# Kernel tuning notes

Hardware: AMD Instinct MI355X
Metric: run time of the kernel (lower is better)

Reference implementation:

```python
import jax, jax.numpy as jnp
import numpy as np

HEADS = 8
EMB = 128

def setup_inputs() -> dict:
    key = jax.random.key(0)
    ks = jax.random.split(key, 5)
    b, t, hin = 4, 128, 1024
    N = 50000
    x = jax.random.normal(ks[0], (b, t, hin), dtype=jnp.float32)
    curiosity_score = jax.random.normal(ks[1], (b, t), dtype=jnp.float32)
    Wq = jax.random.normal(ks[2], (EMB * HEADS, hin), dtype=jnp.float32) * (1.0 / np.sqrt(hin))
    keys = jax.random.normal(ks[3], (N, EMB), dtype=jnp.float32)
    values = jax.random.normal(ks[4], (N,), dtype=jnp.float32)
    return {"x": x, "curiosity_score": curiosity_score, "Wq": Wq, "keys": keys, "values": values}

def reference(x, curiosity_score, Wq, keys, values):
    b, t, hin = x.shape
    h, e = HEADS, EMB
    # query projection (torch Linear, no bias): x @ Wq.T -> (b, t, h*e)
    q = jnp.einsum('bti,oi->bto', x, Wq).reshape(b, t, h, e)
    q = q / (e ** 0.25)
    # scores vs shared offline key bank (N, e); buffer was `heads` identical copies,
    # so broadcasting over h is the same math without materializing repeats.
    scores = jnp.einsum('bthe,ne->bthn', q, keys)          # (b, t, h, N)
    attn = jax.nn.softmax(scores, axis=-1)
    # weighted sum of scalar values; curiosity adds a per-query constant to every
    # value, and since attn rows sum to 1 this equals adding curiosity afterwards.
    out = jnp.einsum('bthn,n->bth', attn, values) + curiosity_score[:, :, None]
    out = out.mean(axis=2)                                  # mean over heads
    return out[:, :, None]                                  # (b, t, 1)
```

## Files before the change

kernel.cpp:

```cpp
#include <hip/hip_runtime.h>

#define NHEADS   8
#define EMB_     128
#define BT_      512
#define HIN_     1024
#define NQ_      4096
#define NKEY_    50000
#define NGRP_REAL_ 3125
#define NGRP_    3200
#define NPAD_    51200
#define NPADKEYS_ 1200.0f
#define GPS_     50
#define NSLICES_ 64

#define PROJB_   512
#define CONVB_   1024

#define QSCALE   (0.29730177875068026f * 1.4426950408889634f)

typedef __attribute__((ext_vector_type(8))) short short8v;
typedef __attribute__((ext_vector_type(4))) float float4v;

#if __has_builtin(__builtin_amdgcn_exp2f)
#define EXP2F(x) __builtin_amdgcn_exp2f(x)
#else
#define EXP2F(x) exp2f(x)
#endif

__device__ __forceinline__ short f2bf(float f) {
  unsigned u = __float_as_uint(f);
  u += 0x7fffu + ((u >> 16) & 1u);
  return (short)(u >> 16);
}

#if __has_builtin(__builtin_amdgcn_cvt_pk_bf16_f32)
typedef __attribute__((ext_vector_type(2))) __bf16 bf16x2;
__device__ __forceinline__ unsigned pk2(float a, float b) {
  bf16x2 r = __builtin_amdgcn_cvt_pk_bf16_f32(a, b);
  union { bf16x2 v; unsigned u; } c; c.v = r; return c.u;
}
#else
__device__ __forceinline__ unsigned pk2(float a, float b) {
  return (unsigned)(unsigned short)f2bf(a) | ((unsigned)(unsigned short)f2bf(b) << 16);
}
#endif

__global__ __launch_bounds__(256) void prep_kernel(
    const float* __restrict__ x, const float* __restrict__ Wq,
    short* __restrict__ qb,
    const float* __restrict__ keys, const float* __restrict__ values,
    short* __restrict__ keys_fr, float* __restrict__ vpad) {
  if (blockIdx.x < PROJB_) {
    const int wave = threadIdx.x >> 6, lane = threadIdx.x & 63;
    const int quad = lane >> 4, ln = lane & 15;
    const int tile = blockIdx.x * 4 + wave;
    const int mt = tile >> 6, ot = tile & 63;
    const float* xrow = x  + (mt * 16 + ln) * HIN_ + quad * 8;
    const float* wrow = Wq + (ot * 16 + ln) * HIN_ + quad * 8;
    float4v d = {0.f, 0.f, 0.f, 0.f};

    float4 xa0 = *(const float4*)(xrow);
    float4 xa1 = *(const float4*)(xrow + 4);
    float4 wa0 = *(const float4*)(wrow);
    float4 wa1 = *(const float4*)(wrow + 4);
    float4 xb0 = *(const float4*)(xrow + 32);
    float4 xb1 = *(const float4*)(xrow + 36);
    float4 wb0 = *(const float4*)(wrow + 32);
    float4 wb1 = *(const float4*)(wrow + 36);

#pragma unroll 1
    for (int k0 = 0; k0 < HIN_; k0 += 64) {
      union { short8v s8; unsigned u[4]; } af, bf;
      af.u[0] = pk2(xa0.x, xa0.y); af.u[1] = pk2(xa0.z, xa0.w);
      af.u[2] = pk2(xa1.x, xa1.y); af.u[3] = pk2(xa1.z, xa1.w);
      bf.u[0] = pk2(wa0.x, wa0.y); bf.u[1] = pk2(wa0.z, wa0.w);
      bf.u[2] = pk2(wa1.x, wa1.y); bf.u[3] = pk2(wa1.z, wa1.w);
      if (k0 + 64 < HIN_) {
        xa0 = *(const float4*)(xrow + k0 + 64);
        xa1 = *(const float4*)(xrow + k0 + 68);
        wa0 = *(const float4*)(wrow + k0 + 64);
        wa1 = *(const float4*)(wrow + k0 + 68);
      }
      d = __builtin_amdgcn_mfma_f32_16x16x32_bf16(af.s8, bf.s8, d, 0, 0, 0);

      af.u[0] = pk2(xb0.x, xb0.y); af.u[1] = pk2(xb0.z, xb0.w);
      af.u[2] = pk2(xb1.x, xb1.y); af.u[3] = pk2(xb1.z, xb1.w);
      bf.u[0] = pk2(wb0.x, wb0.y); bf.u[1] = pk2(wb0.z, wb0.w);
      bf.u[2] = pk2(wb1.x, wb1.y); bf.u[3] = pk2(wb1.z, wb1.w);
      if (k0 + 96 < HIN_) {
        xb0 = *(const float4*)(xrow + k0 + 96);
        xb1 = *(const float4*)(xrow + k0 + 100);
        wb0 = *(const float4*)(wrow + k0 + 96);
        wb1 = *(const float4*)(wrow + k0 + 100);
      }
      d = __builtin_amdgcn_mfma_f32_16x16x32_bf16(af.s8, bf.s8, d, 0, 0, 0);
    }
#pragma unroll
    for (int r2 = 0; r2 < 4; ++r2)
      qb[(mt * 16 + quad * 4 + r2) * HIN_ + ot * 16 + ln] = f2bf(d[r2] * QSCALE);
  } else {
    const int cb = blockIdx.x - PROJB_;
    const int t  = threadIdx.x;
#pragma unroll 1
    for (int g = cb; g < NGRP_; g += CONVB_) {
      if (g < NGRP_REAL_) {
        const float* src = keys + (g * 16 + (t & 15)) * EMB_ + (t >> 4) * 8;
        float4 v0 = ((const float4*)src)[0];
        float4 v1 = ((const float4*)src)[1];
        union { short8v s8; unsigned u[4]; } o;
        o.u[0] = pk2(v0.x, v0.y); o.u[1] = pk2(v0.z, v0.w);
        o.u[2] = pk2(v1.x, v1.y); o.u[3] = pk2(v1.z, v1.w);
        ((short8v*)keys_fr)[g * 256 + t] = o.s8;
        if (t < 16) vpad[g * 16 + t] = values[g * 16 + t];
      } else {
        short8v z = (short8v)0;
        ((short8v*)keys_fr)[g * 256 + t] = z;
        if (t < 16) vpad[g * 16 + t] = 0.f;
      }
    }
  }
}

__global__ __launch_bounds__(256) void attn_kernel(
    const short* __restrict__ qb,
    const short* __restrict__ keys_fr,
    const float* __restrict__ vpad,
    float* __restrict__ partials) {
  const int t     = threadIdx.x;
  const int wave  = t >> 6;
  const int lane  = t & 63;
  const int quad  = lane >> 4;
  const int ln    = lane & 15;
  const int l     = blockIdx.x;
  const int xcd   = l & 7;
  const int j     = l >> 3;
  const int slice = xcd * 8 + (j >> 4);
  const int chunk = j & 15;
  const int qbase = chunk * 256 + wave * 64;
  const int g0    = slice * GPS_;
  const int g1    = g0 + GPS_;

  short8v a[4][4];
#pragma unroll
  for (int sub = 0; sub < 4; ++sub)
#pragma unroll
    for (int ks = 0; ks < 4; ++ks)
      a[sub][ks] = *(const short8v*)(qb + (qbase + sub * 16 + ln) * EMB_ + ks * 32 + quad * 8);

  float lsum[4][4], asum[4][4];
#pragma unroll
  for (int i = 0; i < 4; ++i)
#pragma unroll
    for (int jj = 0; jj < 4; ++jj) { lsum[i][jj] = 0.f; asum[i][jj] = 0.f; }

  short8v bA[4], bB[4];
  float vA, vB;
#pragma unroll
  for (int ks = 0; ks < 4; ++ks)
    bA[ks] = *(const short8v*)(keys_fr + ((g0 * 4 + ks) * 64 + lane) * 8);
  vA = vpad[g0 * 16 + ln];
#pragma unroll
  for (int ks = 0; ks < 4; ++ks)
    bB[ks] = *(const short8v*)(keys_fr + (((g0 + 1) * 4 + ks) * 64 + lane) * 8);
  vB = vpad[(g0 + 1) * 16 + ln];

#pragma unroll 1
  for (int g = g0; g < g1; g += 2) {
    {
      float4v d[4];
#pragma unroll
      for (int sub = 0; sub < 4; ++sub) d[sub] = (float4v){0.f, 0.f, 0.f, 0.f};
      __builtin_amdgcn_s_setprio(1);
#pragma unroll
      for (int ks = 0; ks < 4; ++ks)
#pragma unroll
        for (int sub = 0; sub < 4; ++sub)
          d[sub] = __builtin_amdgcn_mfma_f32_16x16x32_bf16(a[sub][ks], bA[ks], d[sub], 0, 0, 0);
      __builtin_amdgcn_s_setprio(0);
      if (g + 2 < g1) {
#pragma unroll
        for (int ks = 0; ks < 4; ++ks)
          bA[ks] = *(const short8v*)(keys_fr + (((g + 2) * 4 + ks) * 64 + lane) * 8);
      }
      float vv = vA;
      if (g + 2 < g1) vA = vpad[(g + 2) * 16 + ln];
#pragma unroll
      for (int sub = 0; sub < 4; ++sub)
#pragma unroll
        for (int r2 = 0; r2 < 4; ++r2) {
          float p = EXP2F(d[sub][r2]);
          lsum[sub][r2] += p;
          asum[sub][r2] = fmaf(p, vv, asum[sub][r2]);
        }
    }
    {
      float4v d[4];
#pragma unroll
      for (int sub = 0; sub < 4; ++sub) d[sub] = (float4v){0.f, 0.f, 0.f, 0.f};
      __builtin_amdgcn_s_setprio(1);
#pragma unroll
      for (int ks = 0; ks < 4; ++ks)
#pragma unroll
        for (int sub = 0; sub < 4; ++sub)
          d[sub] = __builtin_amdgcn_mfma_f32_16x16x32_bf16(a[sub][ks], bB[ks], d[sub], 0, 0, 0);
      __builtin_amdgcn_s_setprio(0);
      if (g + 3 < g1) {
#pragma unroll
        for (int ks = 0; ks < 4; ++ks)
          bB[ks] = *(const short8v*)(keys_fr + (((g + 3) * 4 + ks) * 64 + lane) * 8);
      }
      float vv = vB;
      if (g + 3 < g1) vB = vpad[(g + 3) * 16 + ln];
#pragma unroll
      for (int sub = 0; sub < 4; ++sub)
#pragma unroll
        for (int r2 = 0; r2 < 4; ++r2) {
          float p = EXP2F(d[sub][r2]);
          lsum[sub][r2] += p;
          asum[sub][r2] = fmaf(p, vv, asum[sub][r2]);
        }
    }
  }

#pragma unroll
  for (int sub = 0; sub < 4; ++sub)
#pragma unroll
    for (int r2 = 0; r2 < 4; ++r2) {
      float L = lsum[sub][r2], A = asum[sub][r2];
#pragma unroll
      for (int m = 1; m < 16; m <<= 1) {
        L += __shfl_xor(L, m, 64);
        A += __shfl_xor(A, m, 64);
      }
      if (ln == 0) {
        int q = qbase + sub * 16 + quad * 4 + r2;
        partials[(q * NSLICES_ + slice) * 2 + 0] = L;
        partials[(q * NSLICES_ + slice) * 2 + 1] = A;
      }
    }
}

__global__ __launch_bounds__(256) void finalize_kernel(
    const float* __restrict__ partials, const float* __restrict__ cur,
    float* __restrict__ out) {
  int tid = blockIdx.x * 256 + threadIdx.x;
  int bt = tid >> 3, h = tid & 7;
  int q = bt * NHEADS + h;
  const float4* p = (const float4*)(partials + q * NSLICES_ * 2);
  float sl = 0.f, sa = 0.f;
#pragma unroll
  for (int i = 0; i < NSLICES_ / 2; ++i) {
    float4 v = p[i];
    sl += v.x + v.z;
    sa += v.y + v.w;
  }
  sl -= NPADKEYS_;
  float r = sa / sl;
  r += __shfl_xor(r, 1, 64);
  r += __shfl_xor(r, 2, 64);
  r += __shfl_xor(r, 4, 64);
  if (h == 0) out[bt] = r * (1.f / NHEADS) + cur[bt];
}

extern "C" void kernel_launch(void* const* d_in, const int* in_sizes, int n_in,
                              void* d_out, int out_size, void* d_ws, size_t ws_size,
                              hipStream_t stream) {
  (void)in_sizes; (void)n_in; (void)out_size; (void)ws_size;
  const float* x      = (const float*)d_in[0];
  const float* cur    = (const float*)d_in[1];
  const float* Wq     = (const float*)d_in[2];
  const float* keys   = (const float*)d_in[3];
  const float* values = (const float*)d_in[4];
  float* out = (float*)d_out;

  char* ws = (char*)d_ws;
  short* keys_fr = (short*)(ws);
  float* vpad    = (float*)(ws + 13107200);
  short* qb      = (short*)(ws + 13312000);
  float* part    = (float*)(ws + 14360576);

  hipLaunchKernelGGL(prep_kernel, dim3(PROJB_ + CONVB_), dim3(256), 0, stream,
                     x, Wq, qb, keys, values, keys_fr, vpad);
  hipLaunchKernelGGL(attn_kernel, dim3(1024), dim3(256), 0, stream,
                     qb, keys_fr, vpad, part);
  hipLaunchKernelGGL(finalize_kernel, dim3(16), dim3(256), 0, stream, part, cur, out);
}
```

Baseline: 175.0 us.

## Compute softmax sums and value-weighted sums with an extra MFMA

The per-element scalar accumulation (lsum += p, asum += p*v) is replaced by a second MFMA. Exponentiated scores from two key groups are packed to bf16 and multiplied by a value fragment whose lanes carry the values split into bf16 hi/lo parts plus a ones-vector for the normalizer. The score MFMA operands are swapped so the output layout feeds this MFMA directly, and the cross-lane shuffle reductions at the end are dropped. This removes VALU FMA work and reductions from the hot loop. In exchange the probabilities are rounded to bf16 before accumulation, which adds precision risk and an extra per-iteration load of the value fragment.

```diff
diff --git a/kernel.cpp b/kernel.cpp
--- a/kernel.cpp
+++ b/kernel.cpp
@@ -8,7 +8,7 @@
 #define NKEY_    50000
 #define NGRP_REAL_ 3125
 #define NGRP_    3200
-#define NPAD_    51200
+#define NPAIR_   1600
 #define NPADKEYS_ 1200.0f
 #define GPS_     50
 #define NSLICES_ 64
@@ -32,6 +32,9 @@
   u += 0x7fffu + ((u >> 16) & 1u);
   return (short)(u >> 16);
 }
+__device__ __forceinline__ float bf2f(short h) {
+  return __uint_as_float(((unsigned)(unsigned short)h) << 16);
+}
 
 #if __has_builtin(__builtin_amdgcn_cvt_pk_bf16_f32)
 typedef __attribute__((ext_vector_type(2))) __bf16 bf16x2;
@@ -41,7 +44,9 @@
 }
 #else
 __device__ __forceinline__ unsigned pk2(float a, float b) {
-  return (unsigned)(unsigned short)f2bf(a) | ((unsigned)(unsigned short)f2bf(b) << 16);
+  unsigned r;
+  asm("v_cvt_pk_bf16_f32 %0, %1, %2" : "=v"(r) : "v"(a), "v"(b));
+  return r;
 }
 #endif
 
@@ -49,7 +54,7 @@
     const float* __restrict__ x, const float* __restrict__ Wq,
     short* __restrict__ qb,
     const float* __restrict__ keys, const float* __restrict__ values,
-    short* __restrict__ keys_fr, float* __restrict__ vpad) {
+    short* __restrict__ keys_fr, short* __restrict__ vfr) {
   if (blockIdx.x < PROJB_) {
     const int wave = threadIdx.x >> 6, lane = threadIdx.x & 63;
     const int quad = lane >> 4, ln = lane & 15;
@@ -111,12 +116,27 @@
         o.u[0] = pk2(v0.x, v0.y); o.u[1] = pk2(v0.z, v0.w);
         o.u[2] = pk2(v1.x, v1.y); o.u[3] = pk2(v1.z, v1.w);
         ((short8v*)keys_fr)[g * 256 + t] = o.s8;
-        if (t < 16) vpad[g * 16 + t] = values[g * 16 + t];
       } else {
         short8v z = (short8v)0;
         ((short8v*)keys_fr)[g * 256 + t] = z;
-        if (t < 16) vpad[g * 16 + t] = 0.f;
       }
+    }
+    const int wi = cb * 256 + t;
+    if (wi < NPAIR_ * 4) {
+      const int pg = wi >> 2, Q = wi & 3;
+      short hi[8], lo[8];
+#pragma unroll
+      for (int e = 0; e < 4; ++e) {
+        int idxE = pg * 32 + Q * 4 + e;
+        int idxO = idxE + 16;
+        float fE = (idxE < NKEY_) ? values[idxE] : 0.f;
+        float fO = (idxO < NKEY_) ? values[idxO] : 0.f;
+        hi[e]     = f2bf(fE); lo[e]     = f2bf(fE - bf2f(hi[e]));
+        hi[4 + e] = f2bf(fO); lo[4 + e] = f2bf(fO - bf2f(hi[4 + e]));
+      }
+      short* dst = vfr + pg * 64 + Q * 16;
+#pragma unroll
+      for (int e = 0; e < 8; ++e) { dst[e] = hi[e]; dst[8 + e] = lo[e]; }
     }
   }
 }
@@ -124,7 +144,7 @@
 __global__ __launch_bounds__(256) void attn_kernel(
     const short* __restrict__ qb,
     const short* __restrict__ keys_fr,
-    const float* __restrict__ vpad,
+    const short* __restrict__ vfr,
     float* __restrict__ partials) {
   const int t     = threadIdx.x;
   const int wave  = t >> 6;
@@ -147,97 +167,94 @@
     for (int ks = 0; ks < 4; ++ks)
       a[sub][ks] = *(const short8v*)(qb + (qbase + sub * 16 + ln) * EMB_ + ks * 32 + quad * 8);
 
-  float lsum[4][4], asum[4][4];
-#pragma unroll
-  for (int i = 0; i < 4; ++i)
-#pragma unroll
-    for (int jj = 0; jj < 4; ++jj) { lsum[i][jj] = 0.f; asum[i][jj] = 0.f; }
+  float4v dpv[4];
+#pragma unroll
+  for (int sub = 0; sub < 4; ++sub) dpv[sub] = (float4v){0.f, 0.f, 0.f, 0.f};
+
+  const bool datalane = (ln == 0) || (ln == 2);
+  const unsigned cvf = (ln == 1) ? 0x3F803F80u : 0u;
+  const unsigned vinv = datalane ? (unsigned)(quad * 16 + (ln == 2 ? 8 : 0)) : 0u;
+  const unsigned dmask = datalane ? 0xFFFFFFFFu : 0u;
 
   short8v bA[4], bB[4];
-  float vA, vB;
 #pragma unroll
   for (int ks = 0; ks < 4; ++ks)
     bA[ks] = *(const short8v*)(keys_fr + ((g0 * 4 + ks) * 64 + lane) * 8);
-  vA = vpad[g0 * 16 + ln];
 #pragma unroll
   for (int ks = 0; ks < 4; ++ks)
     bB[ks] = *(const short8v*)(keys_fr + (((g0 + 1) * 4 + ks) * 64 + lane) * 8);
-  vB = vpad[(g0 + 1) * 16 + ln];
 
 #pragma unroll 1
   for (int g = g0; g < g1; g += 2) {
-    {
-      float4v d[4];
-#pragma unroll
-      for (int sub = 0; sub < 4; ++sub) d[sub] = (float4v){0.f, 0.f, 0.f, 0.f};
-      __builtin_amdgcn_s_setprio(1);
+    union { short8v s8; unsigned u[4]; } vfu, vlu;
+    vlu.s8 = *(const short8v*)(vfr + (vinv + (((unsigned)((g >> 1) * 64)) & dmask)));
+#pragma unroll
+    for (int i = 0; i < 4; ++i) vfu.u[i] = datalane ? vlu.u[i] : cvf;
+
+    float4v dE[4], dO[4];
+#pragma unroll
+    for (int sub = 0; sub < 4; ++sub) dE[sub] = (float4v){0.f, 0.f, 0.f, 0.f};
+    __builtin_amdgcn_s_setprio(1);
+#pragma unroll
+    for (int ks = 0; ks < 4; ++ks)
+#pragma unroll
+      for (int sub = 0; sub < 4; ++sub)
+        dE[sub] = __builtin_amdgcn_mfma_f32_16x16x32_bf16(bA[ks], a[sub][ks], dE[sub], 0, 0, 0);
+    __builtin_amdgcn_s_setprio(0);
+    if (g + 2 < g1) {
 #pragma unroll
       for (int ks = 0; ks < 4; ++ks)
-#pragma unroll
-        for (int sub = 0; sub < 4; ++sub)
-          d[sub] = __builtin_amdgcn_mfma_f32_16x16x32_bf16(a[sub][ks], bA[ks], d[sub], 0, 0, 0);
-      __builtin_amdgcn_s_setprio(0);
-      if (g + 2 < g1) {
-#pragma unroll
-        for (int ks = 0; ks < 4; ++ks)
-          bA[ks] = *(const short8v*)(keys_fr + (((g + 2) * 4 + ks) * 64 + lane) * 8);
-      }
-      float vv = vA;
-      if (g + 2 < g1) vA = vpad[(g + 2) * 16 + ln];
+        bA[ks] = *(const short8v*)(keys_fr + (((g + 2) * 4 + ks) * 64 + lane) * 8);
+    }
+#pragma unroll
+    for (int sub = 0; sub < 4; ++sub)
+#pragma unroll
+      for (int r2 = 0; r2 < 4; ++r2) dE[sub][r2] = EXP2F(dE[sub][r2]);
+    unsigned pbl[4][2];
+#pragma unroll
+    for (int sub = 0; sub < 4; ++sub) {
+      pbl[sub][0] = pk2(dE[sub][0], dE[sub][1]);
+      pbl[sub][1] = pk2(dE[sub][2], dE[sub][3]);
+    }
+
+#pragma unroll
+    for (int sub = 0; sub < 4; ++sub) dO[sub] = (float4v){0.f, 0.f, 0.f, 0.f};
+    __builtin_amdgcn_s_setprio(1);
+#pragma unroll
+    for (int ks = 0; ks < 4; ++ks)
 #pragma unroll
       for (int sub = 0; sub < 4; ++sub)
-#pragma unroll
-        for (int r2 = 0; r2 < 4; ++r2) {
-          float p = EXP2F(d[sub][r2]);
-          lsum[sub][r2] += p;
-          asum[sub][r2] = fmaf(p, vv, asum[sub][r2]);
-        }
-    }
-    {
-      float4v d[4];
-#pragma unroll
-      for (int sub = 0; sub < 4; ++sub) d[sub] = (float4v){0.f, 0.f, 0.f, 0.f};
-      __builtin_amdgcn_s_setprio(1);
+        dO[sub] = __builtin_amdgcn_mfma_f32_16x16x32_bf16(bB[ks], a[sub][ks], dO[sub], 0, 0, 0);
+    __builtin_amdgcn_s_setprio(0);
+    if (g + 3 < g1) {
 #pragma unroll
       for (int ks = 0; ks < 4; ++ks)
-#pragma unroll
-        for (int sub = 0; sub < 4; ++sub)
-          d[sub] = __builtin_amdgcn_mfma_f32_16x16x32_bf16(a[sub][ks], bB[ks], d[sub], 0, 0, 0);
-      __builtin_amdgcn_s_setprio(0);
-      if (g + 3 < g1) {
-#pragma unroll
-        for (int ks = 0; ks < 4; ++ks)
-          bB[ks] = *(const short8v*)(keys_fr + (((g + 3) * 4 + ks) * 64 + lane) * 8);
-      }
-      float vv = vB;
-      if (g + 3 < g1) vB = vpad[(g + 3) * 16 + ln];
-#pragma unroll
-      for (int sub = 0; sub < 4; ++sub)
-#pragma unroll
-        for (int r2 = 0; r2 < 4; ++r2) {
-          float p = EXP2F(d[sub][r2]);
-          lsum[sub][r2] += p;
-          asum[sub][r2] = fmaf(p, vv, asum[sub][r2]);
-        }
+        bB[ks] = *(const short8v*)(keys_fr + (((g + 3) * 4 + ks) * 64 + lane) * 8);
+    }
+#pragma unroll
+    for (int sub = 0; sub < 4; ++sub)
+#pragma unroll
+      for (int r2 = 0; r2 < 4; ++r2) dO[sub][r2] = EXP2F(dO[sub][r2]);
+
+#pragma unroll
+    for (int sub = 0; sub < 4; ++sub) {
+      union { short8v s8; unsigned u[4]; } pb;
+      pb.u[0] = pbl[sub][0];
+      pb.u[1] = pbl[sub][1];
+      pb.u[2] = pk2(dO[sub][0], dO[sub][1]);
+      pb.u[3] = pk2(dO[sub][2], dO[sub][3]);
+      dpv[sub] = __builtin_amdgcn_mfma_f32_16x16x32_bf16(vfu.s8, pb.s8, dpv[sub], 0, 0, 0);
     }
   }
 
-#pragma unroll
-  for (int sub = 0; sub < 4; ++sub)
-#pragma unroll
-    for (int r2 = 0; r2 < 4; ++r2) {
-      float L = lsum[sub][r2], A = asum[sub][r2];
-#pragma unroll
-      for (int m = 1; m < 16; m <<= 1) {
-        L += __shfl_xor(L, m, 64);
-        A += __shfl_xor(A, m, 64);
-      }
-      if (ln == 0) {
-        int q = qbase + sub * 16 + quad * 4 + r2;
-        partials[(q * NSLICES_ + slice) * 2 + 0] = L;
-        partials[(q * NSLICES_ + slice) * 2 + 1] = A;
-      }
-    }
+  if (quad == 0) {
+#pragma unroll
+    for (int sub = 0; sub < 4; ++sub) {
+      int q = qbase + sub * 16 + ln;
+      partials[(q * NSLICES_ + slice) * 2 + 0] = dpv[sub][1];
+      partials[(q * NSLICES_ + slice) * 2 + 1] = dpv[sub][0] + dpv[sub][2];
+    }
+  }
 }
 
 __global__ __launch_bounds__(256) void finalize_kernel(
@@ -275,13 +292,13 @@
 
   char* ws = (char*)d_ws;
   short* keys_fr = (short*)(ws);
-  float* vpad    = (float*)(ws + 13107200);
+  short* vfr     = (short*)(ws + 13107200);
   short* qb      = (short*)(ws + 13312000);
   float* part    = (float*)(ws + 14360576);
 
   hipLaunchKernelGGL(prep_kernel, dim3(PROJB_ + CONVB_), dim3(256), 0, stream,
-                     x, Wq, qb, keys, values, keys_fr, vpad);
+                     x, Wq, qb, keys, values, keys_fr, vfr);
   hipLaunchKernelGGL(attn_kernel, dim3(1024), dim3(256), 0, stream,
-                     qb, keys_fr, vpad, part);
+                     qb, keys_fr, vfr, part);
   hipLaunchKernelGGL(finalize_kernel, dim3(16), dim3(256), 0, stream, part, cur, out);
 }
```

Result: slower. 193.2 us (+10.4%).

## Halve per-wave query tile and fuse even/odd key group MFMA chains

Applied to the files above, without the earlier changes.

Each wave now handles 32 queries instead of 64, so the grid doubles to 2048 blocks and register pressure per wave drops. The two key-group MFMA chains are issued together and their exp/accumulate work is merged into one loop, giving more independent MFMAs in flight. The unused pk2 fallback now uses inline asm for the bf16 convert, and an unused define is dropped. In exchange, key tiles are reloaded by twice as many waves, which raises L2/global traffic per query.

```diff
diff --git a/kernel.cpp b/kernel.cpp
--- a/kernel.cpp
+++ b/kernel.cpp
@@ -8,7 +8,6 @@
 #define NKEY_    50000
 #define NGRP_REAL_ 3125
 #define NGRP_    3200
-#define NPAD_    51200
 #define NPADKEYS_ 1200.0f
 #define GPS_     50
 #define NSLICES_ 64
@@ -41,7 +40,9 @@
 }
 #else
 __device__ __forceinline__ unsigned pk2(float a, float b) {
-  return (unsigned)(unsigned short)f2bf(a) | ((unsigned)(unsigned short)f2bf(b) << 16);
+  unsigned r;
+  asm("v_cvt_pk_bf16_f32 %0, %1, %2" : "=v"(r) : "v"(a), "v"(b));
+  return r;
 }
 #endif
 
@@ -134,24 +135,26 @@
   const int l     = blockIdx.x;
   const int xcd   = l & 7;
   const int j     = l >> 3;
-  const int slice = xcd * 8 + (j >> 4);
-  const int chunk = j & 15;
-  const int qbase = chunk * 256 + wave * 64;
+  const int slice = xcd * 8 + (j >> 5);
+  const int chunk = j & 31;
+  const int qbase = chunk * 128 + wave * 32;
   const int g0    = slice * GPS_;
   const int g1    = g0 + GPS_;
 
-  short8v a[4][4];
-#pragma unroll
-  for (int sub = 0; sub < 4; ++sub)
+  short8v a[2][4];
+#pragma unroll
+  for (int sub = 0; sub < 2; ++sub)
 #pragma unroll
     for (int ks = 0; ks < 4; ++ks)
       a[sub][ks] = *(const short8v*)(qb + (qbase + sub * 16 + ln) * EMB_ + ks * 32 + quad * 8);
 
-  float lsum[4][4], asum[4][4];
-#pragma unroll
-  for (int i = 0; i < 4; ++i)
+  float lsum[2][4], asum[2][4];
+#pragma unroll
+  for (int i = 0; i < 2; ++i)
 #pragma unroll
     for (int jj = 0; jj < 4; ++jj) { lsum[i][jj] = 0.f; asum[i][jj] = 0.f; }
+
+  const float4v z4 = {0.f, 0.f, 0.f, 0.f};
 
   short8v bA[4], bB[4];
   float vA, vB;
@@ -166,64 +169,50 @@
 
 #pragma unroll 1
   for (int g = g0; g < g1; g += 2) {
-    {
-      float4v d[4];
-#pragma unroll
-      for (int sub = 0; sub < 4; ++sub) d[sub] = (float4v){0.f, 0.f, 0.f, 0.f};
-      __builtin_amdgcn_s_setprio(1);
+    float4v dE[2], dO[2];
+    __builtin_amdgcn_s_setprio(1);
+    dE[0] = __builtin_amdgcn_mfma_f32_16x16x32_bf16(a[0][0], bA[0], z4, 0, 0, 0);
+    dE[1] = __builtin_amdgcn_mfma_f32_16x16x32_bf16(a[1][0], bA[0], z4, 0, 0, 0);
+    dO[0] = __builtin_amdgcn_mfma_f32_16x16x32_bf16(a[0][0], bB[0], z4, 0, 0, 0);
+    dO[1] = __builtin_amdgcn_mfma_f32_16x16x32_bf16(a[1][0], bB[0], z4, 0, 0, 0);
+#pragma unroll
+    for (int ks = 1; ks < 4; ++ks) {
+      dE[0] = __builtin_amdgcn_mfma_f32_16x16x32_bf16(a[0][ks], bA[ks], dE[0], 0, 0, 0);
+      dE[1] = __builtin_amdgcn_mfma_f32_16x16x32_bf16(a[1][ks], bA[ks], dE[1], 0, 0, 0);
+      dO[0] = __builtin_amdgcn_mfma_f32_16x16x32_bf16(a[0][ks], bB[ks], dO[0], 0, 0, 0);
+      dO[1] = __builtin_amdgcn_mfma_f32_16x16x32_bf16(a[1][ks], bB[ks], dO[1], 0, 0, 0);
+    }
+    __builtin_amdgcn_s_setprio(0);
+
+    if (g + 2 < g1) {
 #pragma unroll
       for (int ks = 0; ks < 4; ++ks)
-#pragma unroll
-        for (int sub = 0; sub < 4; ++sub)
-          d[sub] = __builtin_amdgcn_mfma_f32_16x16x32_bf16(a[sub][ks], bA[ks], d[sub], 0, 0, 0);
-      __builtin_amdgcn_s_setprio(0);
-      if (g + 2 < g1) {
-#pragma unroll
-        for (int ks = 0; ks < 4; ++ks)
-          bA[ks] = *(const short8v*)(keys_fr + (((g + 2) * 4 + ks) * 64 + lane) * 8);
-      }
-      float vv = vA;
-      if (g + 2 < g1) vA = vpad[(g + 2) * 16 + ln];
-#pragma unroll
-      for (int sub = 0; sub < 4; ++sub)
-#pragma unroll
-        for (int r2 = 0; r2 < 4; ++r2) {
-          float p = EXP2F(d[sub][r2]);
-          lsum[sub][r2] += p;
-          asum[sub][r2] = fmaf(p, vv, asum[sub][r2]);
-        }
-    }
-    {
-      float4v d[4];
-#pragma unroll
-      for (int sub = 0; sub < 4; ++sub) d[sub] = (float4v){0.f, 0.f, 0.f, 0.f};
-      __builtin_amdgcn_s_setprio(1);
+        bA[ks] = *(const short8v*)(keys_fr + (((g + 2) * 4 + ks) * 64 + lane) * 8);
+    }
+    float vvA = vA;
+    if (g + 2 < g1) vA = vpad[(g + 2) * 16 + ln];
+    if (g + 3 < g1) {
 #pragma unroll
       for (int ks = 0; ks < 4; ++ks)
-#pragma unroll
-        for (int sub = 0; sub < 4; ++sub)
-          d[sub] = __builtin_amdgcn_mfma_f32_16x16x32_bf16(a[sub][ks], bB[ks], d[sub], 0, 0, 0);
-      __builtin_amdgcn_s_setprio(0);
-      if (g + 3 < g1) {
-#pragma unroll
-        for (int ks = 0; ks < 4; ++ks)
-          bB[ks] = *(const short8v*)(keys_fr + (((g + 3) * 4 + ks) * 64 + lane) * 8);
-      }
-      float vv = vB;
-      if (g + 3 < g1) vB = vpad[(g + 3) * 16 + ln];
-#pragma unroll
-      for (int sub = 0; sub < 4; ++sub)
-#pragma unroll
-        for (int r2 = 0; r2 < 4; ++r2) {
-          float p = EXP2F(d[sub][r2]);
-          lsum[sub][r2] += p;
-          asum[sub][r2] = fmaf(p, vv, asum[sub][r2]);
-        }
-    }
+        bB[ks] = *(const short8v*)(keys_fr + (((g + 3) * 4 + ks) * 64 + lane) * 8);
+    }
+    float vvB = vB;
+    if (g + 3 < g1) vB = vpad[(g + 3) * 16 + ln];
+
+#pragma unroll
+    for (int sub = 0; sub < 2; ++sub)
+#pragma unroll
+      for (int r2 = 0; r2 < 4; ++r2) {
+        float pE = EXP2F(dE[sub][r2]);
+        float pO = EXP2F(dO[sub][r2]);
+        lsum[sub][r2] += pE + pO;
+        asum[sub][r2] = fmaf(pE, vvA, asum[sub][r2]);
+        asum[sub][r2] = fmaf(pO, vvB, asum[sub][r2]);
+      }
   }
 
 #pragma unroll
-  for (int sub = 0; sub < 4; ++sub)
+  for (int sub = 0; sub < 2; ++sub)
 #pragma unroll
     for (int r2 = 0; r2 < 4; ++r2) {
       float L = lsum[sub][r2], A = asum[sub][r2];
@@ -281,7 +270,7 @@
 
   hipLaunchKernelGGL(prep_kernel, dim3(PROJB_ + CONVB_), dim3(256), 0, stream,
                      x, Wq, qb, keys, values, keys_fr, vpad);
-  hipLaunchKernelGGL(attn_kernel, dim3(1024), dim3(256), 0, stream,
+  hipLaunchKernelGGL(attn_kernel, dim3(2048), dim3(256), 0, stream,
                      qb, keys_fr, vpad, part);
   hipLaunchKernelGGL(finalize_kernel, dim3(16), dim3(256), 0, stream, part, cur, out);
 }
```

Measured after the change: 181.3 us. 1.04x slower.
